# Kernel tuning notes

Hardware: AMD Instinct MI355X
Metric: run time of the kernel (lower is better)

Reference implementation:

```python
import jax, jax.numpy as jnp
import numpy as np

B, T, C, H = 2, 2048, 768, 12
HD = C // H


def setup_inputs() -> dict:
    key = jax.random.key(0)
    ks = jax.random.split(key, 8)
    s = 0.02
    return {
        "x": jax.random.normal(ks[0], (B, T, C), dtype=jnp.float32),
        "attn_mask1": jax.random.randint(ks[1], (B, T), 0, 2, dtype=jnp.int32),
        "Wq": jax.random.normal(ks[2], (C, C), dtype=jnp.float32) * s,
        "bq": jnp.zeros((C,), dtype=jnp.float32),
        "Wk": jax.random.normal(ks[3], (C, C), dtype=jnp.float32) * s,
        "bk": jnp.zeros((C,), dtype=jnp.float32),
        "Wv": jax.random.normal(ks[4], (C, C), dtype=jnp.float32) * s,
        "bv": jnp.zeros((C,), dtype=jnp.float32),
        "Wp": jax.random.normal(ks[5], (C, C), dtype=jnp.float32) * s,
        "bp": jnp.zeros((C,), dtype=jnp.float32),
    }


def reference(x, attn_mask1, Wq, bq, Wk, bk, Wv, bv, Wp, bp):
    b, t, c = x.shape
    # linear projections, split heads -> [B, H, T, HD]
    def heads(w, bias):
        return (x @ w.T + bias).reshape(b, t, H, HD).transpose(0, 2, 1, 3)
    q = heads(Wq, bq)
    k = heads(Wk, bk)
    v = heads(Wv, bv)
    scale = 1.0 / jnp.sqrt(jnp.asarray(HD, dtype=x.dtype))
    att = jnp.einsum("bhqd,bhkd->bhqk", q, k) * scale  # [B,H,T,T]
    # key-padding mask: original tiles [B,T] along the query axis only
    key_mask = (attn_mask1 == 0)[:, None, None, :]  # [B,1,1,T]
    att = jnp.where(key_mask, -jnp.inf, att)
    att = jax.nn.softmax(att, axis=-1)
    y = jnp.einsum("bhqk,bhkd->bhqd", att, v)  # [B,H,T,HD]
    y = y.transpose(0, 2, 1, 3).reshape(b, t, c)
    return y @ Wp.T + bp
```

## Files before the change

kernel.cpp:

```cpp
#include <hip/hip_runtime.h>
#include <stdint.h>

typedef unsigned short u16;
typedef __bf16 bf16x8 __attribute__((ext_vector_type(8)));
typedef float f32x4 __attribute__((ext_vector_type(4)));

#define BB 2
#define TT 2048
#define CC 768
#define HH 12
#define HD 64
#define MTOT (BB*TT)

__device__ __forceinline__ u16 f2bf(float f) {
    uint32_t u = __builtin_bit_cast(uint32_t, f);
    u = (u + 0x7fffu + ((u >> 16) & 1u)) >> 16;
    return (u16)u;
}
__device__ __forceinline__ float bf2f(u16 h) {
    return __builtin_bit_cast(float, (uint32_t)h << 16);
}

union U16x8 { uint4 v; u16 s[8]; };
union BFrag { bf16x8 b; u16 s[8]; };

__global__ void k_cvt(const float* __restrict__ src, u16* __restrict__ dst, int n4) {
    int i = blockIdx.x * blockDim.x + threadIdx.x;
    if (i >= n4) return;
    float4 v = reinterpret_cast<const float4*>(src)[i];
    uint lo = (uint)f2bf(v.x) | ((uint)f2bf(v.y) << 16);
    uint hi = (uint)f2bf(v.z) | ((uint)f2bf(v.w) << 16);
    reinterpret_cast<uint2*>(dst)[i] = make_uint2(lo, hi);
}

__global__ void k_mask(const int* __restrict__ m, float* __restrict__ o, int n) {
    int i = blockIdx.x * blockDim.x + threadIdx.x;
    if (i < n) o[i] = (m[i] == 0) ? -1e30f : 0.0f;
}

#define GBM 128
#define GBN 128
#define GBK 32
#define KLD (GBK + 8)

__global__ __launch_bounds__(256)
void k_gemm(const u16* __restrict__ A, const u16* __restrict__ W,
            const float* __restrict__ bias,
            u16* __restrict__ outHead, float* __restrict__ outLin,
            int M, int N, int K)
{
    __shared__ alignas(16) u16 As[GBM][KLD];
    __shared__ alignas(16) u16 Bs[GBN][KLD];

    const int tid  = threadIdx.x;
    const int lane = tid & 63;
    const int wave = tid >> 6;
    const int m0 = blockIdx.y * GBM;
    const int n0 = blockIdx.x * GBN;
    const int wm = (wave >> 1) * 64;
    const int wn = (wave & 1) * 64;

    f32x4 acc[4][4];
#pragma unroll
    for (int m = 0; m < 4; ++m)
#pragma unroll
        for (int n = 0; n < 4; ++n)
            acc[m][n] = f32x4{0.f, 0.f, 0.f, 0.f};

    const int srow = tid >> 2;
    const int scol = (tid & 3) * 8;

    for (int k0 = 0; k0 < K; k0 += GBK) {
        __syncthreads();
        {
            const u16* ga = A + (size_t)(m0 + srow) * K + k0 + scol;
            *reinterpret_cast<uint4*>(&As[srow][scol]) = *reinterpret_cast<const uint4*>(ga);
            *reinterpret_cast<uint4*>(&As[srow + 64][scol]) =
                *reinterpret_cast<const uint4*>(ga + (size_t)64 * K);
            const u16* gb = W + (size_t)(n0 + srow) * K + k0 + scol;
            *reinterpret_cast<uint4*>(&Bs[srow][scol]) = *reinterpret_cast<const uint4*>(gb);
            *reinterpret_cast<uint4*>(&Bs[srow + 64][scol]) =
                *reinterpret_cast<const uint4*>(gb + (size_t)64 * K);
        }
        __syncthreads();

        bf16x8 af[4], bfb[4];
#pragma unroll
        for (int m = 0; m < 4; ++m)
            af[m] = *reinterpret_cast<const bf16x8*>(&As[wm + m * 16 + (lane & 15)][(lane >> 4) * 8]);
#pragma unroll
        for (int n = 0; n < 4; ++n)
            bfb[n] = *reinterpret_cast<const bf16x8*>(&Bs[wn + n * 16 + (lane & 15)][(lane >> 4) * 8]);
#pragma unroll
        for (int m = 0; m < 4; ++m)
#pragma unroll
            for (int n = 0; n < 4; ++n)
                acc[m][n] = __builtin_amdgcn_mfma_f32_16x16x32_bf16(af[m], bfb[n], acc[m][n], 0, 0, 0);
    }

    const int col   = lane & 15;
    const int rbase = (lane >> 4) * 4;
#pragma unroll
    for (int m = 0; m < 4; ++m) {
#pragma unroll
        for (int n = 0; n < 4; ++n) {
            const int gn = n0 + wn + n * 16 + col;
            const float bv = bias[gn];
#pragma unroll
            for (int j = 0; j < 4; ++j) {
                const int gm = m0 + wm + m * 16 + rbase + j;
                const float val = acc[m][n][j] + bv;
                if (outLin) {
                    outLin[(size_t)gm * N + gn] = val;
                } else {
                    const int h = gn >> 6, hd = gn & 63;
                    const int b = gm >> 11, t = gm & (TT - 1);
                    outHead[((size_t)(b * HH + h) * TT + t) * HD + hd] = f2bf(val);
                }
            }
        }
    }
}

__global__ __launch_bounds__(256)
void k_attn(const u16* __restrict__ Qh, const u16* __restrict__ Kh,
            const u16* __restrict__ Vh, const float* __restrict__ maskb,
            u16* __restrict__ Y)
{
    __shared__ alignas(16) u16 Ks[64][72];
    __shared__ alignas(16) u16 Vt[64][72];
    __shared__ alignas(16) u16 Ps[4][16][72];
    __shared__ float mb[64];

    const int tid  = threadIdx.x;
    const int lane = tid & 63;
    const int wave = tid >> 6;
    const int bh = blockIdx.y;
    const int b  = bh / HH;
    const int h  = bh % HH;
    const int q0 = blockIdx.x * 64 + wave * 16;

    const u16* Qp = Qh + (size_t)bh * TT * HD;
    const u16* Kp = Kh + (size_t)bh * TT * HD;
    const u16* Vp = Vh + (size_t)bh * TT * HD;

    bf16x8 qf[2];
    {
        const int r = q0 + (lane & 15);
#pragma unroll
        for (int ks = 0; ks < 2; ++ks) {
            U16x8 t;
            t.v = *reinterpret_cast<const uint4*>(Qp + (size_t)r * HD + ks * 32 + (lane >> 4) * 8);
            BFrag o;
#pragma unroll
            for (int j = 0; j < 8; ++j) o.s[j] = f2bf(bf2f(t.s[j]) * 0.125f);
            qf[ks] = o.b;
        }
    }

    f32x4 oacc[4];
#pragma unroll
    for (int n = 0; n < 4; ++n) oacc[n] = f32x4{0.f, 0.f, 0.f, 0.f};
    float mrun[4], lrun[4];
#pragma unroll
    for (int j = 0; j < 4; ++j) { mrun[j] = -1e30f; lrun[j] = 0.f; }

    const int srow = tid >> 3;
    const int scol = (tid & 7) * 8;

    for (int kt = 0; kt < TT; kt += 64) {
        __syncthreads();
#pragma unroll
        for (int i = 0; i < 2; ++i) {
            const int r = srow + i * 32;
            *reinterpret_cast<uint4*>(&Ks[r][scol]) =
                *reinterpret_cast<const uint4*>(Kp + (size_t)(kt + r) * HD + scol);
            U16x8 t;
            t.v = *reinterpret_cast<const uint4*>(Vp + (size_t)(kt + r) * HD + scol);
#pragma unroll
            for (int j = 0; j < 8; ++j) Vt[scol + j][r] = t.s[j];
        }
        if (tid < 64) mb[tid] = maskb[b * TT + kt + tid];
        __syncthreads();

        f32x4 sacc[4];
#pragma unroll
        for (int n = 0; n < 4; ++n) sacc[n] = f32x4{0.f, 0.f, 0.f, 0.f};
#pragma unroll
        for (int ks = 0; ks < 2; ++ks)
#pragma unroll
            for (int n = 0; n < 4; ++n) {
                bf16x8 kf = *reinterpret_cast<const bf16x8*>(
                    &Ks[n * 16 + (lane & 15)][ks * 32 + (lane >> 4) * 8]);
                sacc[n] = __builtin_amdgcn_mfma_f32_16x16x32_bf16(qf[ks], kf, sacc[n], 0, 0, 0);
            }

        float p[4][4], tmax[4];
#pragma unroll
        for (int j = 0; j < 4; ++j) tmax[j] = -1e30f;
        float mbv[4];
#pragma unroll
        for (int n = 0; n < 4; ++n) mbv[n] = mb[n * 16 + (lane & 15)];
#pragma unroll
        for (int n = 0; n < 4; ++n)
#pragma unroll
            for (int j = 0; j < 4; ++j) {
                float s = sacc[n][j] + mbv[n];
                p[n][j] = s;
                tmax[j] = fmaxf(tmax[j], s);
            }
#pragma unroll
        for (int off = 1; off < 16; off <<= 1)
#pragma unroll
            for (int j = 0; j < 4; ++j) tmax[j] = fmaxf(tmax[j], __shfl_xor(tmax[j], off));
        float scl[4];
#pragma unroll
        for (int j = 0; j < 4; ++j) {
            float mnew = fmaxf(mrun[j], tmax[j]);
            scl[j] = __expf(mrun[j] - mnew);
            mrun[j] = mnew;
        }
#pragma unroll
        for (int n = 0; n < 4; ++n)
#pragma unroll
            for (int j = 0; j < 4; ++j) {
                float s = p[n][j];
                p[n][j] = (s < -1e29f) ? 0.f : __expf(s - mrun[j]);
            }
#pragma unroll
        for (int j = 0; j < 4; ++j) {
            float s = p[0][j] + p[1][j] + p[2][j] + p[3][j];
#pragma unroll
            for (int off = 1; off < 16; off <<= 1) s += __shfl_xor(s, off);
            lrun[j] = lrun[j] * scl[j] + s;
        }

#pragma unroll
        for (int n = 0; n < 4; ++n)
#pragma unroll
            for (int j = 0; j < 4; ++j)
                Ps[wave][(lane >> 4) * 4 + j][n * 16 + (lane & 15)] = f2bf(p[n][j]);

#pragma unroll
        for (int n = 0; n < 4; ++n)
#pragma unroll
            for (int j = 0; j < 4; ++j) oacc[n][j] *= scl[j];
#pragma unroll
        for (int ks = 0; ks < 2; ++ks) {
            bf16x8 pf = *reinterpret_cast<const bf16x8*>(
                &Ps[wave][lane & 15][ks * 32 + (lane >> 4) * 8]);
#pragma unroll
            for (int n = 0; n < 4; ++n) {
                bf16x8 vf = *reinterpret_cast<const bf16x8*>(
                    &Vt[n * 16 + (lane & 15)][ks * 32 + (lane >> 4) * 8]);
                oacc[n] = __builtin_amdgcn_mfma_f32_16x16x32_bf16(pf, vf, oacc[n], 0, 0, 0);
            }
        }
    }

#pragma unroll
    for (int n = 0; n < 4; ++n)
#pragma unroll
        for (int j = 0; j < 4; ++j) {
            const int t = q0 + (lane >> 4) * 4 + j;
            const int c = h * 64 + n * 16 + (lane & 15);
            Y[((size_t)b * TT + t) * CC + c] = f2bf(oacc[n][j] / lrun[j]);
        }
}

extern "C" void kernel_launch(void* const* d_in, const int* in_sizes, int n_in,
                              void* d_out, int out_size, void* d_ws, size_t ws_size,
                              hipStream_t stream)
{
    const float* x    = (const float*)d_in[0];
    const int*   mask = (const int*)d_in[1];
    const float* Wq   = (const float*)d_in[2];
    const float* bq   = (const float*)d_in[3];
    const float* Wk   = (const float*)d_in[4];
    const float* bk   = (const float*)d_in[5];
    const float* Wv   = (const float*)d_in[6];
    const float* bv   = (const float*)d_in[7];
    const float* Wp   = (const float*)d_in[8];
    const float* bp   = (const float*)d_in[9];
    float* out = (float*)d_out;

    char* w = (char*)d_ws;
    auto alloc = [&](size_t bytes) {
        char* p = w;
        w += (bytes + 255) & ~(size_t)255;
        return p;
    };
    u16* x_bf  = (u16*)alloc((size_t)MTOT * CC * 2);
    u16* wq_bf = (u16*)alloc((size_t)CC * CC * 2);
    u16* wk_bf = (u16*)alloc((size_t)CC * CC * 2);
    u16* wv_bf = (u16*)alloc((size_t)CC * CC * 2);
    u16* wp_bf = (u16*)alloc((size_t)CC * CC * 2);
    u16* qh    = (u16*)alloc((size_t)MTOT * CC * 2);
    u16* kh    = (u16*)alloc((size_t)MTOT * CC * 2);
    u16* vh    = (u16*)alloc((size_t)MTOT * CC * 2);
    u16* y_bf  = (u16*)alloc((size_t)MTOT * CC * 2);
    float* maskb = (float*)alloc((size_t)BB * TT * 4);

    const int NX4 = MTOT * CC / 4;
    k_cvt<<<(NX4 + 255) / 256, 256, 0, stream>>>(x, x_bf, NX4);
    const int NW4 = CC * CC / 4;
    k_cvt<<<(NW4 + 255) / 256, 256, 0, stream>>>(Wq, wq_bf, NW4);
    k_cvt<<<(NW4 + 255) / 256, 256, 0, stream>>>(Wk, wk_bf, NW4);
    k_cvt<<<(NW4 + 255) / 256, 256, 0, stream>>>(Wv, wv_bf, NW4);
    k_cvt<<<(NW4 + 255) / 256, 256, 0, stream>>>(Wp, wp_bf, NW4);
    k_mask<<<(BB * TT + 255) / 256, 256, 0, stream>>>(mask, maskb, BB * TT);

    dim3 gg(CC / GBN, MTOT / GBM);
    k_gemm<<<gg, 256, 0, stream>>>(x_bf, wq_bf, bq, qh, nullptr, MTOT, CC, CC);
    k_gemm<<<gg, 256, 0, stream>>>(x_bf, wk_bf, bk, kh, nullptr, MTOT, CC, CC);
    k_gemm<<<gg, 256, 0, stream>>>(x_bf, wv_bf, bv, vh, nullptr, MTOT, CC, CC);

    k_attn<<<dim3(TT / 64, BB * HH), 256, 0, stream>>>(qh, kh, vh, maskb, y_bf);

    k_gemm<<<gg, 256, 0, stream>>>(y_bf, wp_bf, bp, nullptr, out, MTOT, CC, CC);
}
```

Before: 319.3 us.

## Fuse QKV GEMM, use global_load_lds, and rewrite attention as single-wave blocks

Packs the Q, K and V weights and biases so one GEMM launch produces all three projections, with V written pre-transposed for the attention kernel. The GEMM tile loads now go global-to-LDS directly, with no padding on the LDS arrays. The attention kernel becomes a one-wave block handling 32 queries over 128-key tiles. It reads K and V fragments straight from global memory instead of staging them in shared memory, which drops the barriers, and it remaps block indices for locality. The cost is unpadded LDS that may cause bank conflicts, many uncoalesced global loads in attention, and a scattered transposed V store.

Result: faster. 268.4 us (-15.9%).

```diff
diff --git a/kernel.cpp b/kernel.cpp
--- a/kernel.cpp
+++ b/kernel.cpp
@@ -11,6 +11,7 @@
 #define HH 12
 #define HD 64
 #define MTOT (BB*TT)
+#define N_QKV (3*CC)
 
 __device__ __forceinline__ u16 f2bf(float f) {
     uint32_t u = __builtin_bit_cast(uint32_t, f);
@@ -22,7 +23,12 @@
 }
 
 union U16x8 { uint4 v; u16 s[8]; };
-union BFrag { bf16x8 b; u16 s[8]; };
+
+__device__ __forceinline__ void gl_lds16(const u16* g, u16* l) {
+    __builtin_amdgcn_global_load_lds(
+        (const __attribute__((address_space(1))) uint32_t*)g,
+        (__attribute__((address_space(3))) uint32_t*)l, 16, 0, 0);
+}
 
 __global__ void k_cvt(const float* __restrict__ src, u16* __restrict__ dst, int n4) {
     int i = blockIdx.x * blockDim.x + threadIdx.x;
@@ -38,19 +44,26 @@
     if (i < n) o[i] = (m[i] == 0) ? -1e30f : 0.0f;
 }
 
+__global__ void k_packb(const float* __restrict__ bq, const float* __restrict__ bk,
+                        const float* __restrict__ bv, float* __restrict__ o) {
+    int i = blockIdx.x * blockDim.x + threadIdx.x;
+    if (i < CC) o[i] = bq[i];
+    else if (i < 2 * CC) o[i] = bk[i - CC];
+    else if (i < 3 * CC) o[i] = bv[i - 2 * CC];
+}
+
 #define GBM 128
 #define GBN 128
 #define GBK 32
-#define KLD (GBK + 8)
 
 __global__ __launch_bounds__(256)
 void k_gemm(const u16* __restrict__ A, const u16* __restrict__ W,
-            const float* __restrict__ bias,
-            u16* __restrict__ outHead, float* __restrict__ outLin,
-            int M, int N, int K)
+            const float* __restrict__ bias, int K, int N, int mode,
+            u16* __restrict__ outQ, u16* __restrict__ outK, u16* __restrict__ outVt,
+            float* __restrict__ outLin)
 {
-    __shared__ alignas(16) u16 As[GBM][KLD];
-    __shared__ alignas(16) u16 Bs[GBN][KLD];
+    __shared__ alignas(16) u16 As[GBM][GBK];
+    __shared__ alignas(16) u16 Bs[GBN][GBK];
 
     const int tid  = threadIdx.x;
     const int lane = tid & 63;
@@ -67,20 +80,17 @@
         for (int n = 0; n < 4; ++n)
             acc[m][n] = f32x4{0.f, 0.f, 0.f, 0.f};
 
-    const int srow = tid >> 2;
-    const int scol = (tid & 3) * 8;
+    const int lrow = lane >> 2;
+    const int lcol = (lane & 3) * 8;
 
     for (int k0 = 0; k0 < K; k0 += GBK) {
         __syncthreads();
         {
-            const u16* ga = A + (size_t)(m0 + srow) * K + k0 + scol;
-            *reinterpret_cast<uint4*>(&As[srow][scol]) = *reinterpret_cast<const uint4*>(ga);
-            *reinterpret_cast<uint4*>(&As[srow + 64][scol]) =
-                *reinterpret_cast<const uint4*>(ga + (size_t)64 * K);
-            const u16* gb = W + (size_t)(n0 + srow) * K + k0 + scol;
-            *reinterpret_cast<uint4*>(&Bs[srow][scol]) = *reinterpret_cast<const uint4*>(gb);
-            *reinterpret_cast<uint4*>(&Bs[srow + 64][scol]) =
-                *reinterpret_cast<const uint4*>(gb + (size_t)64 * K);
+            const int r0 = wave * 32;
+            gl_lds16(A + (size_t)(m0 + r0 + lrow) * K + k0 + lcol,      &As[r0][0]);
+            gl_lds16(A + (size_t)(m0 + r0 + 16 + lrow) * K + k0 + lcol, &As[r0 + 16][0]);
+            gl_lds16(W + (size_t)(n0 + r0 + lrow) * K + k0 + lcol,      &Bs[r0][0]);
+            gl_lds16(W + (size_t)(n0 + r0 + 16 + lrow) * K + k0 + lcol, &Bs[r0 + 16][0]);
         }
         __syncthreads();
 
@@ -110,162 +120,204 @@
             for (int j = 0; j < 4; ++j) {
                 const int gm = m0 + wm + m * 16 + rbase + j;
                 const float val = acc[m][n][j] + bv;
-                if (outLin) {
+                if (mode == 1) {
                     outLin[(size_t)gm * N + gn] = val;
                 } else {
-                    const int h = gn >> 6, hd = gn & 63;
+                    const int proj = gn / CC;
+                    const int c = gn - proj * CC;
+                    const int h = c >> 6, hd = c & 63;
                     const int b = gm >> 11, t = gm & (TT - 1);
-                    outHead[((size_t)(b * HH + h) * TT + t) * HD + hd] = f2bf(val);
+                    if (proj == 0)
+                        outQ[((size_t)(b * HH + h) * TT + t) * HD + hd] = f2bf(val);
+                    else if (proj == 1)
+                        outK[((size_t)(b * HH + h) * TT + t) * HD + hd] = f2bf(val);
+                    else
+                        outVt[((size_t)(b * HH + h) * HD + hd) * TT + t] = f2bf(val);
                 }
             }
         }
     }
 }
 
-__global__ __launch_bounds__(256)
+__global__ __launch_bounds__(64)
 void k_attn(const u16* __restrict__ Qh, const u16* __restrict__ Kh,
-            const u16* __restrict__ Vh, const float* __restrict__ maskb,
+            const u16* __restrict__ Vt, const float* __restrict__ maskb,
             u16* __restrict__ Y)
 {
-    __shared__ alignas(16) u16 Ks[64][72];
-    __shared__ alignas(16) u16 Vt[64][72];
-    __shared__ alignas(16) u16 Ps[4][16][72];
-    __shared__ float mb[64];
-
-    const int tid  = threadIdx.x;
-    const int lane = tid & 63;
-    const int wave = tid >> 6;
-    const int bh = blockIdx.y;
-    const int b  = bh / HH;
-    const int h  = bh % HH;
-    const int q0 = blockIdx.x * 64 + wave * 16;
+    __shared__ alignas(16) u16 Ps[32][136];
+
+    const int lane = threadIdx.x;
+    const int raw  = blockIdx.x;
+    const int virt = (raw & 7) * 192 + (raw >> 3);
+    const int bh = virt >> 6;
+    const int b  = bh / HH, h = bh % HH;
+    const int q0 = (virt & 63) * 32;
 
     const u16* Qp = Qh + (size_t)bh * TT * HD;
     const u16* Kp = Kh + (size_t)bh * TT * HD;
-    const u16* Vp = Vh + (size_t)bh * TT * HD;
-
-    bf16x8 qf[2];
-    {
-        const int r = q0 + (lane & 15);
+    const u16* Vp = Vt + (size_t)bh * HD * TT;
+    const float* mrow = maskb + b * TT;
+
+    const int l15 = lane & 15;
+    const int lg  = lane >> 4;
+
+    bf16x8 qf[2][2];
+#pragma unroll
+    for (int m = 0; m < 2; ++m)
 #pragma unroll
         for (int ks = 0; ks < 2; ++ks) {
             U16x8 t;
-            t.v = *reinterpret_cast<const uint4*>(Qp + (size_t)r * HD + ks * 32 + (lane >> 4) * 8);
-            BFrag o;
+            t.v = *reinterpret_cast<const uint4*>(
+                Qp + (size_t)(q0 + m * 16 + l15) * HD + ks * 32 + lg * 8);
+            U16x8 o;
 #pragma unroll
             for (int j = 0; j < 8; ++j) o.s[j] = f2bf(bf2f(t.s[j]) * 0.125f);
-            qf[ks] = o.b;
+            qf[m][ks] = __builtin_bit_cast(bf16x8, o.v);
+        }
+
+    f32x4 oacc[2][4];
+#pragma unroll
+    for (int m = 0; m < 2; ++m)
+#pragma unroll
+        for (int n = 0; n < 4; ++n) oacc[m][n] = f32x4{0.f, 0.f, 0.f, 0.f};
+    float mrun[2][4], lrun[2][4];
+#pragma unroll
+    for (int m = 0; m < 2; ++m)
+#pragma unroll
+        for (int j = 0; j < 4; ++j) { mrun[m][j] = -1e30f; lrun[m][j] = 0.f; }
+
+    for (int kt = 0; kt < TT; kt += 128) {
+        f32x4 sacc[2][8];
+#pragma unroll
+        for (int m = 0; m < 2; ++m)
+#pragma unroll
+            for (int n = 0; n < 8; ++n) sacc[m][n] = f32x4{0.f, 0.f, 0.f, 0.f};
+#pragma unroll
+        for (int ks = 0; ks < 2; ++ks) {
+            uint4 kfr[8];
+#pragma unroll
+            for (int n = 0; n < 8; ++n)
+                kfr[n] = *reinterpret_cast<const uint4*>(
+                    Kp + (size_t)(kt + n * 16 + l15) * HD + ks * 32 + lg * 8);
+#pragma unroll
+            for (int n = 0; n < 8; ++n) {
+                bf16x8 kf = __builtin_bit_cast(bf16x8, kfr[n]);
+#pragma unroll
+                for (int m = 0; m < 2; ++m)
+                    sacc[m][n] = __builtin_amdgcn_mfma_f32_16x16x32_bf16(qf[m][ks], kf, sacc[m][n], 0, 0, 0);
+            }
+        }
+
+        float mbv[8];
+#pragma unroll
+        for (int n = 0; n < 8; ++n) mbv[n] = mrow[kt + n * 16 + l15];
+
+        float tmax[2][4];
+#pragma unroll
+        for (int m = 0; m < 2; ++m)
+#pragma unroll
+            for (int j = 0; j < 4; ++j) tmax[m][j] = -1e30f;
+#pragma unroll
+        for (int m = 0; m < 2; ++m)
+#pragma unroll
+            for (int n = 0; n < 8; ++n)
+#pragma unroll
+                for (int j = 0; j < 4; ++j) {
+                    float s = sacc[m][n][j] + mbv[n];
+                    sacc[m][n][j] = s;
+                    tmax[m][j] = fmaxf(tmax[m][j], s);
+                }
+#pragma unroll
+        for (int off = 1; off < 16; off <<= 1)
+#pragma unroll
+            for (int m = 0; m < 2; ++m)
+#pragma unroll
+                for (int j = 0; j < 4; ++j)
+                    tmax[m][j] = fmaxf(tmax[m][j], __shfl_xor(tmax[m][j], off));
+
+        float scl[2][4];
+#pragma unroll
+        for (int m = 0; m < 2; ++m)
+#pragma unroll
+            for (int j = 0; j < 4; ++j) {
+                float mnew = fmaxf(mrun[m][j], tmax[m][j]);
+                scl[m][j] = __expf(mrun[m][j] - mnew);
+                mrun[m][j] = mnew;
+            }
+
+        float rs[2][4];
+#pragma unroll
+        for (int m = 0; m < 2; ++m)
+#pragma unroll
+            for (int j = 0; j < 4; ++j) rs[m][j] = 0.f;
+#pragma unroll
+        for (int m = 0; m < 2; ++m)
+#pragma unroll
+            for (int n = 0; n < 8; ++n)
+#pragma unroll
+                for (int j = 0; j < 4; ++j) {
+                    float s = sacc[m][n][j];
+                    float p = (s < -1e29f) ? 0.f : __expf(s - mrun[m][j]);
+                    sacc[m][n][j] = p;
+                    rs[m][j] += p;
+                }
+#pragma unroll
+        for (int off = 1; off < 16; off <<= 1)
+#pragma unroll
+            for (int m = 0; m < 2; ++m)
+#pragma unroll
+                for (int j = 0; j < 4; ++j) rs[m][j] += __shfl_xor(rs[m][j], off);
+#pragma unroll
+        for (int m = 0; m < 2; ++m)
+#pragma unroll
+            for (int j = 0; j < 4; ++j) lrun[m][j] = lrun[m][j] * scl[m][j] + rs[m][j];
+
+#pragma unroll
+        for (int m = 0; m < 2; ++m)
+#pragma unroll
+            for (int n = 0; n < 8; ++n)
+#pragma unroll
+                for (int j = 0; j < 4; ++j)
+                    Ps[m * 16 + lg * 4 + j][n * 16 + l15] = f2bf(sacc[m][n][j]);
+
+#pragma unroll
+        for (int m = 0; m < 2; ++m)
+#pragma unroll
+            for (int n = 0; n < 4; ++n)
+#pragma unroll
+                for (int j = 0; j < 4; ++j) oacc[m][n][j] *= scl[m][j];
+
+#pragma unroll
+        for (int ks2 = 0; ks2 < 4; ++ks2) {
+            bf16x8 pf[2];
+#pragma unroll
+            for (int m = 0; m < 2; ++m)
+                pf[m] = *reinterpret_cast<const bf16x8*>(&Ps[m * 16 + l15][ks2 * 32 + lg * 8]);
+            uint4 vfr[4];
+#pragma unroll
+            for (int n = 0; n < 4; ++n)
+                vfr[n] = *reinterpret_cast<const uint4*>(
+                    Vp + (size_t)(n * 16 + l15) * TT + kt + ks2 * 32 + lg * 8);
+#pragma unroll
+            for (int n = 0; n < 4; ++n) {
+                bf16x8 vf = __builtin_bit_cast(bf16x8, vfr[n]);
+#pragma unroll
+                for (int m = 0; m < 2; ++m)
+                    oacc[m][n] = __builtin_amdgcn_mfma_f32_16x16x32_bf16(pf[m], vf, oacc[m][n], 0, 0, 0);
+            }
         }
     }
 
-    f32x4 oacc[4];
-#pragma unroll
-    for (int n = 0; n < 4; ++n) oacc[n] = f32x4{0.f, 0.f, 0.f, 0.f};
-    float mrun[4], lrun[4];
-#pragma unroll
-    for (int j = 0; j < 4; ++j) { mrun[j] = -1e30f; lrun[j] = 0.f; }
-
-    const int srow = tid >> 3;
-    const int scol = (tid & 7) * 8;
-
-    for (int kt = 0; kt < TT; kt += 64) {
-        __syncthreads();
-#pragma unroll
-        for (int i = 0; i < 2; ++i) {
-            const int r = srow + i * 32;
-            *reinterpret_cast<uint4*>(&Ks[r][scol]) =
-                *reinterpret_cast<const uint4*>(Kp + (size_t)(kt + r) * HD + scol);
-            U16x8 t;
-            t.v = *reinterpret_cast<const uint4*>(Vp + (size_t)(kt + r) * HD + scol);
-#pragma unroll
-            for (int j = 0; j < 8; ++j) Vt[scol + j][r] = t.s[j];
-        }
-        if (tid < 64) mb[tid] = maskb[b * TT + kt + tid];
-        __syncthreads();
-
-        f32x4 sacc[4];
-#pragma unroll
-        for (int n = 0; n < 4; ++n) sacc[n] = f32x4{0.f, 0.f, 0.f, 0.f};
-#pragma unroll
-        for (int ks = 0; ks < 2; ++ks)
-#pragma unroll
-            for (int n = 0; n < 4; ++n) {
-                bf16x8 kf = *reinterpret_cast<const bf16x8*>(
-                    &Ks[n * 16 + (lane & 15)][ks * 32 + (lane >> 4) * 8]);
-                sacc[n] = __builtin_amdgcn_mfma_f32_16x16x32_bf16(qf[ks], kf, sacc[n], 0, 0, 0);
-            }
-
-        float p[4][4], tmax[4];
-#pragma unroll
-        for (int j = 0; j < 4; ++j) tmax[j] = -1e30f;
-        float mbv[4];
-#pragma unroll
-        for (int n = 0; n < 4; ++n) mbv[n] = mb[n * 16 + (lane & 15)];
+#pragma unroll
+    for (int m = 0; m < 2; ++m)
 #pragma unroll
         for (int n = 0; n < 4; ++n)
 #pragma unroll
             for (int j = 0; j < 4; ++j) {
-                float s = sacc[n][j] + mbv[n];
-                p[n][j] = s;
-                tmax[j] = fmaxf(tmax[j], s);
-            }
-#pragma unroll
-        for (int off = 1; off < 16; off <<= 1)
-#pragma unroll
-            for (int j = 0; j < 4; ++j) tmax[j] = fmaxf(tmax[j], __shfl_xor(tmax[j], off));
-        float scl[4];
-#pragma unroll
-        for (int j = 0; j < 4; ++j) {
-            float mnew = fmaxf(mrun[j], tmax[j]);
-            scl[j] = __expf(mrun[j] - mnew);
-            mrun[j] = mnew;
-        }
-#pragma unroll
-        for (int n = 0; n < 4; ++n)
-#pragma unroll
-            for (int j = 0; j < 4; ++j) {
-                float s = p[n][j];
-                p[n][j] = (s < -1e29f) ? 0.f : __expf(s - mrun[j]);
-            }
-#pragma unroll
-        for (int j = 0; j < 4; ++j) {
-            float s = p[0][j] + p[1][j] + p[2][j] + p[3][j];
-#pragma unroll
-            for (int off = 1; off < 16; off <<= 1) s += __shfl_xor(s, off);
-            lrun[j] = lrun[j] * scl[j] + s;
-        }
-
-#pragma unroll
-        for (int n = 0; n < 4; ++n)
-#pragma unroll
-            for (int j = 0; j < 4; ++j)
-                Ps[wave][(lane >> 4) * 4 + j][n * 16 + (lane & 15)] = f2bf(p[n][j]);
-
-#pragma unroll
-        for (int n = 0; n < 4; ++n)
-#pragma unroll
-            for (int j = 0; j < 4; ++j) oacc[n][j] *= scl[j];
-#pragma unroll
-        for (int ks = 0; ks < 2; ++ks) {
-            bf16x8 pf = *reinterpret_cast<const bf16x8*>(
-                &Ps[wave][lane & 15][ks * 32 + (lane >> 4) * 8]);
-#pragma unroll
-            for (int n = 0; n < 4; ++n) {
-                bf16x8 vf = *reinterpret_cast<const bf16x8*>(
-                    &Vt[n * 16 + (lane & 15)][ks * 32 + (lane >> 4) * 8]);
-                oacc[n] = __builtin_amdgcn_mfma_f32_16x16x32_bf16(pf, vf, oacc[n], 0, 0, 0);
-            }
-        }
-    }
-
-#pragma unroll
-    for (int n = 0; n < 4; ++n)
-#pragma unroll
-        for (int j = 0; j < 4; ++j) {
-            const int t = q0 + (lane >> 4) * 4 + j;
-            const int c = h * 64 + n * 16 + (lane & 15);
-            Y[((size_t)b * TT + t) * CC + c] = f2bf(oacc[n][j] / lrun[j]);
-        }
+                const int t = q0 + m * 16 + lg * 4 + j;
+                const int c = h * 64 + n * 16 + l15;
+                Y[((size_t)b * TT + t) * CC + c] = f2bf(oacc[m][n][j] / lrun[m][j]);
+            }
 }
 
 extern "C" void kernel_launch(void* const* d_in, const int* in_sizes, int n_in,
@@ -290,32 +342,31 @@
         w += (bytes + 255) & ~(size_t)255;
         return p;
     };
-    u16* x_bf  = (u16*)alloc((size_t)MTOT * CC * 2);
-    u16* wq_bf = (u16*)alloc((size_t)CC * CC * 2);
-    u16* wk_bf = (u16*)alloc((size_t)CC * CC * 2);
-    u16* wv_bf = (u16*)alloc((size_t)CC * CC * 2);
-    u16* wp_bf = (u16*)alloc((size_t)CC * CC * 2);
-    u16* qh    = (u16*)alloc((size_t)MTOT * CC * 2);
-    u16* kh    = (u16*)alloc((size_t)MTOT * CC * 2);
-    u16* vh    = (u16*)alloc((size_t)MTOT * CC * 2);
-    u16* y_bf  = (u16*)alloc((size_t)MTOT * CC * 2);
+    u16* x_bf    = (u16*)alloc((size_t)MTOT * CC * 2);
+    u16* wqkv_bf = (u16*)alloc((size_t)3 * CC * CC * 2);
+    u16* wp_bf   = (u16*)alloc((size_t)CC * CC * 2);
+    u16* qh      = (u16*)alloc((size_t)MTOT * CC * 2);
+    u16* kh      = (u16*)alloc((size_t)MTOT * CC * 2);
+    u16* vt      = (u16*)alloc((size_t)MTOT * CC * 2);
+    u16* y_bf    = (u16*)alloc((size_t)MTOT * CC * 2);
     float* maskb = (float*)alloc((size_t)BB * TT * 4);
+    float* bqkv  = (float*)alloc((size_t)N_QKV * 4);
 
     const int NX4 = MTOT * CC / 4;
     k_cvt<<<(NX4 + 255) / 256, 256, 0, stream>>>(x, x_bf, NX4);
     const int NW4 = CC * CC / 4;
-    k_cvt<<<(NW4 + 255) / 256, 256, 0, stream>>>(Wq, wq_bf, NW4);
-    k_cvt<<<(NW4 + 255) / 256, 256, 0, stream>>>(Wk, wk_bf, NW4);
-    k_cvt<<<(NW4 + 255) / 256, 256, 0, stream>>>(Wv, wv_bf, NW4);
+    k_cvt<<<(NW4 + 255) / 256, 256, 0, stream>>>(Wq, wqkv_bf, NW4);
+    k_cvt<<<(NW4 + 255) / 256, 256, 0, stream>>>(Wk, wqkv_bf + (size_t)CC * CC, NW4);
+    k_cvt<<<(NW4 + 255) / 256, 256, 0, stream>>>(Wv, wqkv_bf + (size_t)2 * CC * CC, NW4);
     k_cvt<<<(NW4 + 255) / 256, 256, 0, stream>>>(Wp, wp_bf, NW4);
     k_mask<<<(BB * TT + 255) / 256, 256, 0, stream>>>(mask, maskb, BB * TT);
-
-    dim3 gg(CC / GBN, MTOT / GBM);
-    k_gemm<<<gg, 256, 0, stream>>>(x_bf, wq_bf, bq, qh, nullptr, MTOT, CC, CC);
-    k_gemm<<<gg, 256, 0, stream>>>(x_bf, wk_bf, bk, kh, nullptr, MTOT, CC, CC);
-    k_gemm<<<gg, 256, 0, stream>>>(x_bf, wv_bf, bv, vh, nullptr, MTOT, CC, CC);
-
-    k_attn<<<dim3(TT / 64, BB * HH), 256, 0, stream>>>(qh, kh, vh, maskb, y_bf);
-
-    k_gemm<<<gg, 256, 0, stream>>>(y_bf, wp_bf, bp, nullptr, out, MTOT, CC, CC);
-}
+    k_packb<<<(N_QKV + 255) / 256, 256, 0, stream>>>(bq, bk, bv, bqkv);
+
+    k_gemm<<<dim3(N_QKV / GBN, MTOT / GBM), 256, 0, stream>>>(
+        x_bf, wqkv_bf, bqkv, CC, N_QKV, 0, qh, kh, vt, nullptr);
+
+    k_attn<<<dim3(1536), 64, 0, stream>>>(qh, kh, vt, maskb, y_bf);
+
+    k_gemm<<<dim3(CC / GBN, MTOT / GBM), 256, 0, stream>>>(
+        y_bf, wp_bf, bp, CC, CC, 1, nullptr, nullptr, nullptr, out);
+}
```
